# Kernel tuning notes

Hardware: AMD Instinct MI355X
Metric: run time of the kernel (lower is better)

## Reference

```python
import jax, jax.numpy as jnp
import numpy as np

NEG = -1000000000.0

def setup_inputs() -> dict:
    key = jax.random.key(0)
    k1, k2 = jax.random.split(key)
    N, D, K = 8192, 4096, 64
    z = jax.random.normal(k1, (N, D), dtype=jnp.float32)
    W = jax.random.normal(k2, (K, D), dtype=jnp.float32) * (1.0 / np.sqrt(D))
    b = jnp.zeros((K,), dtype=jnp.float32)
    return {"z": z, "W": W, "b": b, "k": 2}

def reference(z, W, b, k):
    # logits: [N, K]
    logits = jnp.einsum('nd,kd->nk', z, W) + b
    _, topk_idx = jax.lax.top_k(logits, k)  # [N, k]
    N = logits.shape[0]
    rows = jnp.arange(N)[:, None]
    mask = jnp.zeros_like(logits).at[rows, topk_idx].set(1.0)
    sparse_logits = logits + NEG * (1.0 - mask)
    alpha = jax.nn.softmax(sparse_logits, axis=-1)
    return alpha
```

## Files before the change

### kernel.cpp

```cpp
#include <hip/hip_runtime.h>
#include <math.h>


typedef _Float16 f16x8 __attribute__((ext_vector_type(8)));
typedef _Float16 f16x4 __attribute__((ext_vector_type(4)));
typedef float    f32x4 __attribute__((ext_vector_type(4)));

constexpr int D_DIM  = 4096;
constexpr int K_DIM  = 64;
constexpr int BM     = 64;
constexpr int CH     = 64;
constexpr int KQ     = 4;
constexpr int KRANGE = D_DIM / KQ;
constexpr int NCH    = KRANGE / CH;
constexpr int BLOCK  = 512;
constexpr int LSTR   = 72;

__global__ __launch_bounds__(BLOCK, 4) void gemm_f16limb(
    const float* __restrict__ z, const float* __restrict__ W,
    float* __restrict__ part, int N)
{
    __shared__ __align__(16) _Float16 Az[2][BM][LSTR];
    __shared__ __align__(16) _Float16 Bw[2][K_DIM][LSTR];

    const int tid  = threadIdx.x;
    const int lane = tid & 63;
    const int wv   = tid >> 6;
    const int mt   = wv >> 1;
    const int nh   = wv & 1;
    const int m16  = lane & 15;
    const int quad = lane >> 4;

    const int rgrp  = blockIdx.x >> 2;
    const int kq    = blockIdx.x & 3;
    const long m0   = (long)rgrp * BM;
    const int kbase = kq * KRANGE;

    float4 zb[2], wb[2];
#pragma unroll
    for (int i = 0; i < 2; ++i) {
        int f = tid + i * BLOCK, r = f >> 4, k4 = (f & 15) * 4;
        zb[i] = *(const float4*)(z + (m0 + r) * (long)D_DIM + kbase + k4);
        wb[i] = *(const float4*)(W + (long)r * D_DIM + kbase + k4);
    }

    f32x4 acch[2], accl[2];
#pragma unroll
    for (int t = 0; t < 2; ++t) {
        acch[t] = (f32x4){0.f, 0.f, 0.f, 0.f};
        accl[t] = (f32x4){0.f, 0.f, 0.f, 0.f};
    }

    for (int ch = 0; ch < NCH; ++ch) {
#pragma unroll
        for (int i = 0; i < 2; ++i) {
            int f = tid + i * BLOCK, r = f >> 4, k4 = (f & 15) * 4;
            const float* pz = (const float*)&zb[i];
            const float* pw = (const float*)&wb[i];
            f16x4 zh, zl, wh, wl;
#pragma unroll
            for (int j = 0; j < 4; ++j) {
                _Float16 h = (_Float16)pz[j];
                zh[j] = h;
                zl[j] = (_Float16)((pz[j] - (float)h) * 2048.0f);
                _Float16 g = (_Float16)pw[j];
                wh[j] = g;
                wl[j] = (_Float16)((pw[j] - (float)g) * 2048.0f);
            }
            *(f16x4*)&Az[0][r][k4] = zh;
            *(f16x4*)&Az[1][r][k4] = zl;
            *(f16x4*)&Bw[0][r][k4] = wh;
            *(f16x4*)&Bw[1][r][k4] = wl;
        }
        __syncthreads();

        if (ch + 1 < NCH) {
            const int k0 = kbase + (ch + 1) * CH;
#pragma unroll
            for (int i = 0; i < 2; ++i) {
                int f = tid + i * BLOCK, r = f >> 4, k4 = (f & 15) * 4;
                zb[i] = *(const float4*)(z + (m0 + r) * (long)D_DIM + k0 + k4);
                wb[i] = *(const float4*)(W + (long)r * D_DIM + k0 + k4);
            }
        }

        const int mrow = mt * 16 + m16;
#pragma unroll
        for (int ks = 0; ks < 2; ++ks) {
            const int ko = ks * 32 + quad * 8;
            const f16x8 ah = *(const f16x8*)&Az[0][mrow][ko];
            const f16x8 al = *(const f16x8*)&Az[1][mrow][ko];
#pragma unroll
            for (int t = 0; t < 2; ++t) {
                const int ncol = (nh * 2 + t) * 16 + m16;
                const f16x8 bh = *(const f16x8*)&Bw[0][ncol][ko];
                const f16x8 bl = *(const f16x8*)&Bw[1][ncol][ko];
                accl[t] = __builtin_amdgcn_mfma_f32_16x16x32_f16(al, bh, accl[t], 0, 0, 0);
                accl[t] = __builtin_amdgcn_mfma_f32_16x16x32_f16(ah, bl, accl[t], 0, 0, 0);
                acch[t] = __builtin_amdgcn_mfma_f32_16x16x32_f16(ah, bh, acch[t], 0, 0, 0);
            }
        }
        __syncthreads();
    }

#pragma unroll
    for (int t = 0; t < 2; ++t) {
#pragma unroll
        for (int r = 0; r < 4; ++r) {
            long row = m0 + mt * 16 + quad * 4 + r;
            int  col = (nh * 2 + t) * 16 + m16;
            part[((long)kq * N + row) * K_DIM + col] =
                acch[t][r] + accl[t][r] * 4.8828125e-4f;
        }
    }
}

constexpr int RG2  = 32;
constexpr int BLK2 = 256;

__global__ __launch_bounds__(BLK2) void reduce_topk(
    const float* __restrict__ part, const float* __restrict__ bias,
    float* __restrict__ out, int N)
{
    __shared__ float lg[RG2][K_DIM + 1];
    __shared__ float sa1[RG2], sa2[RG2];
    __shared__ int   si1[RG2], si2[RG2];

    const int tid = threadIdx.x;
    const long r0 = (long)blockIdx.x * RG2;

#pragma unroll
    for (int i = 0; i < (RG2 * K_DIM) / (BLK2 * 4); ++i) {
        int f = tid + i * BLK2, r = f >> 4, c4 = (f & 15) * 4;
        float4 s = *(const float4*)(part + (r0 + r) * K_DIM + c4);
#pragma unroll
        for (int q = 1; q < KQ; ++q) {
            const float4 v = *(const float4*)(part + ((long)q * N + r0 + r) * K_DIM + c4);
            s.x += v.x; s.y += v.y; s.z += v.z; s.w += v.w;
        }
        const float4 bv = *(const float4*)(bias + c4);
        lg[r][c4 + 0] = s.x + bv.x;
        lg[r][c4 + 1] = s.y + bv.y;
        lg[r][c4 + 2] = s.z + bv.z;
        lg[r][c4 + 3] = s.w + bv.w;
    }
    __syncthreads();

    if (tid < RG2) {
        float m1 = -INFINITY, m2 = -INFINITY;
        int i1 = 0, i2 = 0;
        for (int j = 0; j < K_DIM; ++j) {
            float v = lg[tid][j];
            if (v > m1)      { m2 = m1; i2 = i1; m1 = v; i1 = j; }
            else if (v > m2) { m2 = v; i2 = j; }
        }
        float e2  = expf(m2 - m1);
        float inv = 1.f / (1.f + e2);
        sa1[tid] = inv; sa2[tid] = e2 * inv;
        si1[tid] = i1;  si2[tid] = i2;
    }
    __syncthreads();

    float* obase = out + r0 * K_DIM;
#pragma unroll
    for (int i = 0; i < (RG2 * K_DIM) / (BLK2 * 4); ++i) {
        int f = tid + i * BLK2, r = f >> 4, j = (f & 15) * 4;
        int i1 = si1[r], i2 = si2[r];
        float a1 = sa1[r], a2 = sa2[r];
        float4 v;
        v.x = (j + 0 == i1) ? a1 : ((j + 0 == i2) ? a2 : 0.f);
        v.y = (j + 1 == i1) ? a1 : ((j + 1 == i2) ? a2 : 0.f);
        v.z = (j + 2 == i1) ? a1 : ((j + 2 == i2) ? a2 : 0.f);
        v.w = (j + 3 == i1) ? a1 : ((j + 3 == i2) ? a2 : 0.f);
        *(float4*)(obase + (long)r * K_DIM + j) = v;
    }
}

extern "C" void kernel_launch(void* const* d_in, const int* in_sizes, int n_in,
                              void* d_out, int out_size, void* d_ws, size_t ws_size,
                              hipStream_t stream) {
    const float* z = (const float*)d_in[0];
    const float* W = (const float*)d_in[1];
    const float* b = (const float*)d_in[2];
    float* out  = (float*)d_out;
    float* part = (float*)d_ws;
    const int N = in_sizes[0] / D_DIM;
    gemm_f16limb<<<dim3((N / BM) * KQ), dim3(BLOCK), 0, stream>>>(z, W, part, N);
    reduce_topk <<<dim3(N / RG2),       dim3(BLK2), 0, stream>>>(part, b, out, N);
}
```

Measured before the change: 212.4 us.

## Pre-split W into fp16 limbs once and read them directly from global memory

A new prep kernel converts W into high and low fp16 limb arrays in workspace once per call. The GEMM then loads the W fragments directly from global memory into registers instead of converting them and staging them through LDS in every block. It also doubles the K split to 8 and the chunk size to 128, and raises the occupancy hint in launch bounds. This removes the redundant per-block conversion work on W and halves LDS traffic. In exchange it adds an extra kernel launch, per-MFMA global or L2 loads of W, and twice as many partial sums for the reduction kernel to read.

```diff
diff --git a/kernel.cpp b/kernel.cpp
--- a/kernel.cpp
+++ b/kernel.cpp
@@ -9,19 +9,36 @@
 constexpr int D_DIM  = 4096;
 constexpr int K_DIM  = 64;
 constexpr int BM     = 64;
-constexpr int CH     = 64;
-constexpr int KQ     = 4;
+constexpr int CH     = 128;
+constexpr int KQ     = 8;
 constexpr int KRANGE = D_DIM / KQ;
 constexpr int NCH    = KRANGE / CH;
 constexpr int BLOCK  = 512;
-constexpr int LSTR   = 72;
-
-__global__ __launch_bounds__(BLOCK, 4) void gemm_f16limb(
-    const float* __restrict__ z, const float* __restrict__ W,
-    float* __restrict__ part, int N)
+constexpr int LSTR   = 136;
+
+__global__ __launch_bounds__(256) void prep_w(
+    const float* __restrict__ W, _Float16* __restrict__ Wf0,
+    _Float16* __restrict__ Wf1)
+{
+    int f = blockIdx.x * 256 + threadIdx.x;
+    const float4 v = *(const float4*)(W + (long)f * 4);
+    const float* p = (const float*)&v;
+    f16x4 h, l;
+#pragma unroll
+    for (int j = 0; j < 4; ++j) {
+        _Float16 hh = (_Float16)p[j];
+        h[j] = hh;
+        l[j] = (_Float16)((p[j] - (float)hh) * 2048.0f);
+    }
+    *(f16x4*)(Wf0 + (long)f * 4) = h;
+    *(f16x4*)(Wf1 + (long)f * 4) = l;
+}
+
+__global__ __launch_bounds__(BLOCK, 6) void gemm_f16limb(
+    const float* __restrict__ z, const _Float16* __restrict__ Wf0,
+    const _Float16* __restrict__ Wf1, float* __restrict__ part, int N)
 {
     __shared__ __align__(16) _Float16 Az[2][BM][LSTR];
-    __shared__ __align__(16) _Float16 Bw[2][K_DIM][LSTR];
 
     const int tid  = threadIdx.x;
     const int lane = tid & 63;
@@ -31,17 +48,16 @@
     const int m16  = lane & 15;
     const int quad = lane >> 4;
 
-    const int rgrp  = blockIdx.x >> 2;
-    const int kq    = blockIdx.x & 3;
+    const int rgrp  = blockIdx.x >> 3;
+    const int kq    = blockIdx.x & 7;
     const long m0   = (long)rgrp * BM;
     const int kbase = kq * KRANGE;
 
-    float4 zb[2], wb[2];
-#pragma unroll
-    for (int i = 0; i < 2; ++i) {
-        int f = tid + i * BLOCK, r = f >> 4, k4 = (f & 15) * 4;
-        zb[i] = *(const float4*)(z + (m0 + r) * (long)D_DIM + kbase + k4);
-        wb[i] = *(const float4*)(W + (long)r * D_DIM + kbase + k4);
+    float4 zb[4];
+#pragma unroll
+    for (int i = 0; i < 4; ++i) {
+        int f = tid + i * BLOCK, r = f >> 5, c4 = (f & 31) * 4;
+        zb[i] = *(const float4*)(z + (m0 + r) * (long)D_DIM + kbase + c4);
     }
 
     f32x4 acch[2], accl[2];
@@ -53,48 +69,41 @@
 
     for (int ch = 0; ch < NCH; ++ch) {
 #pragma unroll
-        for (int i = 0; i < 2; ++i) {
-            int f = tid + i * BLOCK, r = f >> 4, k4 = (f & 15) * 4;
-            const float* pz = (const float*)&zb[i];
-            const float* pw = (const float*)&wb[i];
-            f16x4 zh, zl, wh, wl;
+        for (int i = 0; i < 4; ++i) {
+            int f = tid + i * BLOCK, r = f >> 5, c4 = (f & 31) * 4;
+            const float* p = (const float*)&zb[i];
+            f16x4 h, l;
 #pragma unroll
             for (int j = 0; j < 4; ++j) {
-                _Float16 h = (_Float16)pz[j];
-                zh[j] = h;
-                zl[j] = (_Float16)((pz[j] - (float)h) * 2048.0f);
-                _Float16 g = (_Float16)pw[j];
-                wh[j] = g;
-                wl[j] = (_Float16)((pw[j] - (float)g) * 2048.0f);
+                _Float16 hh = (_Float16)p[j];
+                h[j] = hh;
+                l[j] = (_Float16)((p[j] - (float)hh) * 2048.0f);
             }
-            *(f16x4*)&Az[0][r][k4] = zh;
-            *(f16x4*)&Az[1][r][k4] = zl;
-            *(f16x4*)&Bw[0][r][k4] = wh;
-            *(f16x4*)&Bw[1][r][k4] = wl;
-        }
-        __syncthreads();
-
+            *(f16x4*)&Az[0][r][c4] = h;
+            *(f16x4*)&Az[1][r][c4] = l;
+        }
         if (ch + 1 < NCH) {
             const int k0 = kbase + (ch + 1) * CH;
 #pragma unroll
-            for (int i = 0; i < 2; ++i) {
-                int f = tid + i * BLOCK, r = f >> 4, k4 = (f & 15) * 4;
-                zb[i] = *(const float4*)(z + (m0 + r) * (long)D_DIM + k0 + k4);
-                wb[i] = *(const float4*)(W + (long)r * D_DIM + k0 + k4);
+            for (int i = 0; i < 4; ++i) {
+                int f = tid + i * BLOCK, r = f >> 5, c4 = (f & 31) * 4;
+                zb[i] = *(const float4*)(z + (m0 + r) * (long)D_DIM + k0 + c4);
             }
         }
+        __syncthreads();
 
         const int mrow = mt * 16 + m16;
 #pragma unroll
-        for (int ks = 0; ks < 2; ++ks) {
-            const int ko = ks * 32 + quad * 8;
-            const f16x8 ah = *(const f16x8*)&Az[0][mrow][ko];
-            const f16x8 al = *(const f16x8*)&Az[1][mrow][ko];
+        for (int ks2 = 0; ks2 < 4; ++ks2) {
+            const int klocal = ks2 * 32 + quad * 8;
+            const long kglob = kbase + ch * CH + klocal;
+            const f16x8 ah = *(const f16x8*)&Az[0][mrow][klocal];
+            const f16x8 al = *(const f16x8*)&Az[1][mrow][klocal];
 #pragma unroll
             for (int t = 0; t < 2; ++t) {
-                const int ncol = (nh * 2 + t) * 16 + m16;
-                const f16x8 bh = *(const f16x8*)&Bw[0][ncol][ko];
-                const f16x8 bl = *(const f16x8*)&Bw[1][ncol][ko];
+                const int n = (nh * 2 + t) * 16 + m16;
+                const f16x8 bh = *(const f16x8*)(Wf0 + (long)n * D_DIM + kglob);
+                const f16x8 bl = *(const f16x8*)(Wf1 + (long)n * D_DIM + kglob);
                 accl[t] = __builtin_amdgcn_mfma_f32_16x16x32_f16(al, bh, accl[t], 0, 0, 0);
                 accl[t] = __builtin_amdgcn_mfma_f32_16x16x32_f16(ah, bl, accl[t], 0, 0, 0);
                 acch[t] = __builtin_amdgcn_mfma_f32_16x16x32_f16(ah, bh, acch[t], 0, 0, 0);
@@ -183,8 +192,13 @@
     const float* W = (const float*)d_in[1];
     const float* b = (const float*)d_in[2];
     float* out  = (float*)d_out;
-    float* part = (float*)d_ws;
     const int N = in_sizes[0] / D_DIM;
-    gemm_f16limb<<<dim3((N / BM) * KQ), dim3(BLOCK), 0, stream>>>(z, W, part, N);
+
+    float*    part = (float*)d_ws;
+    _Float16* Wf0  = (_Float16*)((char*)d_ws + ((size_t)24 << 20));
+    _Float16* Wf1  = Wf0 + (size_t)K_DIM * D_DIM;
+
+    prep_w      <<<dim3((K_DIM * D_DIM / 4) / 256), dim3(256), 0, stream>>>(W, Wf0, Wf1);
+    gemm_f16limb<<<dim3((N / BM) * KQ), dim3(BLOCK), 0, stream>>>(z, Wf0, Wf1, part, N);
     reduce_topk <<<dim3(N / RG2),       dim3(BLK2), 0, stream>>>(part, b, out, N);
 }
```

New measurement: 256.2 us. +20.6%, slower.
